# Optimization experiments

Measured on AMD Instinct MI355X. Metric: run time of the kernel, lower is better.

Reference implementation:

```python
import jax, jax.numpy as jnp
import numpy as np

B, T, D, P, M = 4, 1024, 512, 64, 256


def setup_inputs() -> dict:
    key = jax.random.key(0)
    ks = jax.random.split(key, 10)
    s_d = 1.0 / np.sqrt(D)
    s_m = 1.0 / np.sqrt(M)
    s_p = 1.0 / np.sqrt(P)
    return {
        "inputs": jax.random.normal(ks[0], (B, T, D), dtype=jnp.float32),
        "ec": jax.random.normal(ks[1], (B, M), dtype=jnp.float32),
        "W1": jax.random.uniform(ks[2], (D, P), jnp.float32, -s_d, s_d),
        "b1": jax.random.uniform(ks[3], (P,), jnp.float32, -s_d, s_d),
        "W2": jax.random.uniform(ks[4], (D, P), jnp.float32, -s_d, s_d),
        "b2": jax.random.uniform(ks[5], (P,), jnp.float32, -s_d, s_d),
        "W3": jax.random.uniform(ks[6], (M, P), jnp.float32, -s_m, s_m),
        "b3": jax.random.uniform(ks[7], (P,), jnp.float32, -s_m, s_m),
        "wa_w": jax.random.uniform(ks[8], (P,), jnp.float32, -s_p, s_p),
        "wa_b": jax.random.uniform(ks[9], (), jnp.float32, -s_p, s_p),
    }


def reference(inputs, ec, W1, b1, W2, b2, W3, b3, wa_w, wa_b):
    # inputs: (B,T,D), ec: (B,M)
    w1h = inputs @ W1 + b1          # (B,T,P)
    w2h = inputs @ W2 + b2          # (B,T,P)
    w3e = ec @ W3 + b3              # (B,P)
    # Gt: (B,T,T,P) via broadcast add + tanh
    gt = jnp.tanh(w1h[:, :, None, :] + w2h[:, None, :, :] + w3e[:, None, None, :])
    at = jnp.einsum('btup,p->btu', gt, wa_w) + wa_b   # (B,T,T)
    at = jax.nn.softmax(at, axis=-1)
    out = jnp.einsum('btu,bud->btd', at, inputs)      # (B,T,D)
    return out
```

## Files before the change

kernel.cpp:

```cpp
#include <hip/hip_runtime.h>
#include <hip/hip_bf16.h>

constexpr int BB = 4;
constexpr int TT = 1024;
constexpr int DD = 512;
constexpr int PP = 64;
constexpr int MM = 256;

constexpr float CSCALE = 2.8853900817779268f;
constexpr float L2E = 1.4426950408889634f;

typedef __attribute__((ext_vector_type(8))) short v8s;
typedef __attribute__((ext_vector_type(4))) float v4f;
typedef __attribute__((ext_vector_type(2))) float v2f;
typedef unsigned int __attribute__((address_space(1))) gu32;
typedef unsigned int __attribute__((address_space(3))) su32;

__device__ __forceinline__ unsigned short f2bf(float f) {
    unsigned u = __builtin_bit_cast(unsigned, f);
    unsigned r = (u + 0x7fffu + ((u >> 16) & 1u)) >> 16;
    return (unsigned short)r;
}
__device__ __forceinline__ float bf2f(unsigned short h) {
    return __builtin_bit_cast(float, (unsigned)h << 16);
}
__device__ __forceinline__ void split2(float v, unsigned short& h, unsigned short& l) {
    unsigned short hh = f2bf(v);
    h = hh;
    l = f2bf(v - bf2f(hh));
}
__device__ __forceinline__ void gld_lds16(const void* g, void* l) {
    __builtin_amdgcn_global_load_lds((const gu32*)g, (su32*)l, 16, 0, 0);
}
__device__ __forceinline__ v2f pfma(v2f a, v2f b, v2f c) {
    return __builtin_elementwise_fma(a, b, c);
}

__global__ __launch_bounds__(256) void prep1_kernel(
    const float* __restrict__ x, const float* __restrict__ ec,
    const float* __restrict__ W1, const float* __restrict__ W2,
    const float* __restrict__ W3, const float* __restrict__ b3,
    unsigned short* __restrict__ xt,
    unsigned short* __restrict__ WhT, unsigned short* __restrict__ WlT,
    float* __restrict__ E3) {
    __shared__ float tile[64][65];
    int bid = blockIdx.x;
    int tid = threadIdx.x;
    if (bid < 512) {
        int d0 = (bid & 7) << 6;
        int u0 = ((bid >> 3) & 15) << 6;
        int b = bid >> 7;
        int c4 = (tid & 15) << 2, r = tid >> 4;
        #pragma unroll
        for (int i = 0; i < 4; i++) {
            int row = r + (i << 4);
            float4 v = *(const float4*)(x + ((size_t)b * TT + u0 + row) * DD + d0 + c4);
            tile[row][c4 + 0] = v.x;
            tile[row][c4 + 1] = v.y;
            tile[row][c4 + 2] = v.z;
            tile[row][c4 + 3] = v.w;
        }
        __syncthreads();
        int dd = tid >> 2;
        int uq = (tid & 3) << 4;
        unsigned short us[16];
        #pragma unroll
        for (int j = 0; j < 16; j++) us[j] = f2bf(tile[uq + j][dd]);
        uint4 w0, w1;
        w0.x = us[0] | ((unsigned)us[1] << 16);  w0.y = us[2] | ((unsigned)us[3] << 16);
        w0.z = us[4] | ((unsigned)us[5] << 16);  w0.w = us[6] | ((unsigned)us[7] << 16);
        w1.x = us[8] | ((unsigned)us[9] << 16);  w1.y = us[10] | ((unsigned)us[11] << 16);
        w1.z = us[12] | ((unsigned)us[13] << 16); w1.w = us[14] | ((unsigned)us[15] << 16);
        unsigned short* dst = xt + ((size_t)b * DD + d0 + dd) * TT + u0 + uq;
        *(uint4*)dst = w0;
        *(uint4*)(dst + 8) = w1;
    } else if (bid < 528) {
        int w = bid - 512;
        int n = tid >> 1;
        int kb = (w << 5) + ((tid & 1) << 4);
        unsigned short hs[16], ls[16];
        #pragma unroll
        for (int kk = 0; kk < 16; kk++) {
            int k = kb + kk;
            float v = (n < 64) ? W1[k * PP + n] : W2[k * PP + (n - 64)];
            split2(v, hs[kk], ls[kk]);
        }
        uint4 a, bqq;
        a.x = hs[0] | ((unsigned)hs[1] << 16);   a.y = hs[2] | ((unsigned)hs[3] << 16);
        a.z = hs[4] | ((unsigned)hs[5] << 16);   a.w = hs[6] | ((unsigned)hs[7] << 16);
        bqq.x = hs[8] | ((unsigned)hs[9] << 16); bqq.y = hs[10] | ((unsigned)hs[11] << 16);
        bqq.z = hs[12] | ((unsigned)hs[13] << 16); bqq.w = hs[14] | ((unsigned)hs[15] << 16);
        *(uint4*)(WhT + (size_t)n * DD + kb) = a;
        *(uint4*)(WhT + (size_t)n * DD + kb + 8) = bqq;
        a.x = ls[0] | ((unsigned)ls[1] << 16);   a.y = ls[2] | ((unsigned)ls[3] << 16);
        a.z = ls[4] | ((unsigned)ls[5] << 16);   a.w = ls[6] | ((unsigned)ls[7] << 16);
        bqq.x = ls[8] | ((unsigned)ls[9] << 16); bqq.y = ls[10] | ((unsigned)ls[11] << 16);
        bqq.z = ls[12] | ((unsigned)ls[13] << 16); bqq.w = ls[14] | ((unsigned)ls[15] << 16);
        *(uint4*)(WlT + (size_t)n * DD + kb) = a;
        *(uint4*)(WlT + (size_t)n * DD + kb + 8) = bqq;
    } else {
        int b = tid >> 6, p = tid & 63;
        float a = b3[p];
        const float* e = ec + (size_t)b * MM;
        #pragma unroll 4
        for (int m = 0; m < MM; m++) a = fmaf(e[m], W3[m * PP + p], a);
        E3[b * PP + p] = __builtin_amdgcn_exp2f(a * CSCALE);
    }
}

__global__ __launch_bounds__(256) void prep2_kernel(
    const float* __restrict__ x,
    const unsigned short* __restrict__ WhT, const unsigned short* __restrict__ WlT,
    const float* __restrict__ b1, const float* __restrict__ b2,
    float* __restrict__ E1, float* __restrict__ E2) {
    __shared__ unsigned short AsH[16][72];
    __shared__ unsigned short AsL[16][72];
    __shared__ unsigned short BsH[128][72];
    __shared__ unsigned short BsL[128][72];
    int m0 = blockIdx.x << 4;
    int tid = threadIdx.x;
    int lane = tid & 63;
    int wv = tid >> 6;
    int wn = wv << 5;
    int l15 = lane & 15;
    int quad = lane >> 4;

    v4f acc[2];
    acc[0] = (v4f){0.f, 0.f, 0.f, 0.f};
    acc[1] = acc[0];

    for (int k0 = 0; k0 < DD; k0 += 64) {
        __syncthreads();
        {
            int row = tid >> 4, k4 = (tid & 15) << 2;
            float4 v = *(const float4*)(x + (size_t)(m0 + row) * DD + k0 + k4);
            unsigned short h0, h1, h2, h3, l0, l1, l2, l3;
            split2(v.x, h0, l0); split2(v.y, h1, l1);
            split2(v.z, h2, l2); split2(v.w, h3, l3);
            uint2 hw, lw;
            hw.x = h0 | ((unsigned)h1 << 16); hw.y = h2 | ((unsigned)h3 << 16);
            lw.x = l0 | ((unsigned)l1 << 16); lw.y = l2 | ((unsigned)l3 << 16);
            *(uint2*)&AsH[row][k4] = hw;
            *(uint2*)&AsL[row][k4] = lw;
        }
        #pragma unroll
        for (int i = 0; i < 4; i++) {
            int s = (i << 8) + tid;
            int row = s >> 3, k8 = (s & 7) << 3;
            *(uint4*)&BsH[row][k8] = *(const uint4*)(WhT + (size_t)row * DD + k0 + k8);
            *(uint4*)&BsL[row][k8] = *(const uint4*)(WlT + (size_t)row * DD + k0 + k8);
        }
        __syncthreads();
        #pragma unroll
        for (int kk = 0; kk < 64; kk += 32) {
            int kc = kk + (quad << 3);
            v8s aH0 = *(const v8s*)&AsH[l15][kc];
            v8s aL0 = *(const v8s*)&AsL[l15][kc];
            #pragma unroll
            for (int nt = 0; nt < 2; nt++) {
                v8s bH = *(const v8s*)&BsH[wn + (nt << 4) + l15][kc];
                v8s bL = *(const v8s*)&BsL[wn + (nt << 4) + l15][kc];
                acc[nt] = __builtin_amdgcn_mfma_f32_16x16x32_bf16(aH0, bH, acc[nt], 0, 0, 0);
                acc[nt] = __builtin_amdgcn_mfma_f32_16x16x32_bf16(aH0, bL, acc[nt], 0, 0, 0);
                acc[nt] = __builtin_amdgcn_mfma_f32_16x16x32_bf16(aL0, bH, acc[nt], 0, 0, 0);
            }
        }
    }
    #pragma unroll
    for (int nt = 0; nt < 2; nt++) {
        int n = wn + (nt << 4) + l15;
        int p = n & 63;
        float bias = (n < 64) ? b1[p] : b2[p];
        float* E = (n < 64) ? E1 : E2;
        int rbase = m0 + (quad << 2);
        #pragma unroll
        for (int r = 0; r < 4; r++) {
            float h = acc[nt][r] + bias;
            E[(size_t)(rbase + r) * PP + p] = __builtin_amdgcn_exp2f(h * CSCALE);
        }
    }
}

__global__ __launch_bounds__(256, 4) void scores_kernel(
    const float* __restrict__ E1, const float* __restrict__ E2,
    const float* __restrict__ E3, const float* __restrict__ wa_w,
    const float* __restrict__ wa_b, unsigned short* __restrict__ at_bf) {
    __shared__ float sm[4][4];
    __shared__ float sl[4][4];
    int tid = threadIdx.x;
    int bid = blockIdx.x;
    int b = bid >> 8;
    int t0 = (bid & 255) << 2;
    int pp = tid & 7;
    int uu = tid >> 3;
    int p0 = pp << 3;
    int lane = tid & 63;
    int wv = tid >> 6;
    int my_i = pp & 3;
    bool pbit1 = (pp & 2) != 0;
    bool pbit0 = (pp & 1) != 0;

    v2f ww2p[8];
    v2f Hp[2][8];
    float base;
    {
        float4 wv0 = *(const float4*)(wa_w + p0);
        float4 wv1 = *(const float4*)(wa_w + p0 + 4);
        float s = wv0.x + wv0.y + wv0.z + wv0.w + wv1.x + wv1.y + wv1.z + wv1.w;
        s += __shfl_xor(s, 1, 64);
        s += __shfl_xor(s, 2, 64);
        s += __shfl_xor(s, 4, 64);
        base = (s + wa_b[0]) * L2E;
        float ww2[8];
        ww2[0] = -2.f * L2E * wv0.x; ww2[1] = -2.f * L2E * wv0.y;
        ww2[2] = -2.f * L2E * wv0.z; ww2[3] = -2.f * L2E * wv0.w;
        ww2[4] = -2.f * L2E * wv1.x; ww2[5] = -2.f * L2E * wv1.y;
        ww2[6] = -2.f * L2E * wv1.z; ww2[7] = -2.f * L2E * wv1.w;
        #pragma unroll
        for (int j = 0; j < 8; j++) ww2p[j] = (v2f){ww2[j], ww2[j]};
        float4 e3a = *(const float4*)(E3 + (b << 6) + p0);
        float4 e3b = *(const float4*)(E3 + (b << 6) + p0 + 4);
        float H[4][8];
        #pragma unroll
        for (int i = 0; i < 4; i++) {
            const float* e1p = E1 + (((size_t)(b << 10) + t0 + i) << 6) + p0;
            float4 a = *(const float4*)e1p;
            float4 c = *(const float4*)(e1p + 4);
            H[i][0] = a.x * e3a.x; H[i][1] = a.y * e3a.y; H[i][2] = a.z * e3a.z; H[i][3] = a.w * e3a.w;
            H[i][4] = c.x * e3b.x; H[i][5] = c.y * e3b.y; H[i][6] = c.z * e3b.z; H[i][7] = c.w * e3b.w;
        }
        #pragma unroll
        for (int pr = 0; pr < 2; pr++)
            #pragma unroll
            for (int j = 0; j < 8; j++)
                Hp[pr][j] = (v2f){H[2 * pr][j], H[2 * pr + 1][j]};
    }
    const v2f one2 = (v2f){1.0f, 1.0f};

    float own[32];
    float mown = -1e30f;
    #pragma unroll
    for (int k = 0; k < 32; k++) {
        int u = (k << 5) + uu;
        const float* ep = E2 + (((size_t)(b << 10) + u) << 6) + p0;
        float4 e0 = *(const float4*)ep;
        float4 e1 = *(const float4*)(ep + 4);
        v2f evp[8];
        evp[0] = (v2f){e0.x, e0.x}; evp[1] = (v2f){e0.y, e0.y};
        evp[2] = (v2f){e0.z, e0.z}; evp[3] = (v2f){e0.w, e0.w};
        evp[4] = (v2f){e1.x, e1.x}; evp[5] = (v2f){e1.y, e1.y};
        evp[6] = (v2f){e1.z, e1.z}; evp[7] = (v2f){e1.w, e1.w};
        float sr_[4];
        #pragma unroll
        for (int pr = 0; pr < 2; pr++) {
            v2f d0 = pfma(Hp[pr][0], evp[0], one2);
            v2f d1 = pfma(Hp[pr][1], evp[1], one2);
            v2f d2 = pfma(Hp[pr][2], evp[2], one2);
            v2f d3 = pfma(Hp[pr][3], evp[3], one2);
            v2f d4 = pfma(Hp[pr][4], evp[4], one2);
            v2f d5 = pfma(Hp[pr][5], evp[5], one2);
            v2f d6 = pfma(Hp[pr][6], evp[6], one2);
            v2f d7 = pfma(Hp[pr][7], evp[7], one2);
            v2f e01 = d0 * d1, e23 = d2 * d3, e45 = d4 * d5, e67 = d6 * d7;
            v2f n01 = pfma(ww2p[0], d1, ww2p[1] * d0);
            v2f n23 = pfma(ww2p[2], d3, ww2p[3] * d2);
            v2f n45 = pfma(ww2p[4], d5, ww2p[5] * d4);
            v2f n67 = pfma(ww2p[6], d7, ww2p[7] * d6);
            v2f q03 = e01 * e23, q47 = e45 * e67;
            v2f n03 = pfma(n23, e01, n01 * e23);
            v2f n47 = pfma(n67, e45, n45 * e67);
            v2f Dq = q03 * q47;
            v2f Nq = pfma(n47, q03, n03 * q47);
            sr_[2 * pr]     = Nq.x * __builtin_amdgcn_rcpf(Dq.x);
            sr_[2 * pr + 1] = Nq.y * __builtin_amdgcn_rcpf(Dq.y);
        }
        float s0 = sr_[0], s1 = sr_[1], s2 = sr_[2], s3 = sr_[3];
        s0 += __shfl_xor(s0, 4, 64);
        s1 += __shfl_xor(s1, 4, 64);
        s2 += __shfl_xor(s2, 4, 64);
        s3 += __shfl_xor(s3, 4, 64);
        float op0 = pbit1 ? s2 : s0;
        float op1 = pbit1 ? s3 : s1;
        float ot0 = pbit1 ? s0 : s2;
        float ot1 = pbit1 ? s1 : s3;
        op0 += __shfl_xor(ot0, 2, 64);
        op1 += __shfl_xor(ot1, 2, 64);
        float osel = pbit0 ? op1 : op0;
        float osnd = pbit0 ? op0 : op1;
        osel += __shfl_xor(osnd, 1, 64);
        float o = osel + base;
        own[k] = o;
        mown = fmaxf(mown, o);
    }
    mown = fmaxf(mown, __shfl_xor(mown, 8, 64));
    mown = fmaxf(mown, __shfl_xor(mown, 16, 64));
    mown = fmaxf(mown, __shfl_xor(mown, 32, 64));
    if (lane < 4) sm[wv][lane] = mown;
    __syncthreads();
    float mx = fmaxf(fmaxf(sm[0][my_i], sm[1][my_i]), fmaxf(sm[2][my_i], sm[3][my_i]));

    float l = 0.f;
    #pragma unroll
    for (int k = 0; k < 32; k++) {
        float e = __builtin_amdgcn_exp2f(own[k] - mx);
        own[k] = e;
        l += e;
    }
    l += __shfl_xor(l, 8, 64);
    l += __shfl_xor(l, 16, 64);
    l += __shfl_xor(l, 32, 64);
    if (lane < 4) sl[wv][lane] = l;
    __syncthreads();
    float inv = 1.0f / (sl[0][my_i] + sl[1][my_i] + sl[2][my_i] + sl[3][my_i]);

    if (pp < 4) {
        size_t rowbase = ((size_t)((b << 10) + t0 + my_i)) << 10;
        #pragma unroll
        for (int k = 0; k < 32; k++) {
            at_bf[rowbase + (k << 5) + uu] = f2bf(own[k] * inv);
        }
    }
}

__global__ __launch_bounds__(256) void av_mfma_kernel(
    const unsigned short* __restrict__ at_bf, const unsigned short* __restrict__ xt,
    float* __restrict__ out) {
    __shared__ unsigned short As[64 * 64];
    __shared__ unsigned short Bs[64 * 64];
    int b = blockIdx.z;
    int m0 = blockIdx.y << 6;
    int n0 = blockIdx.x << 6;
    const unsigned short* A = at_bf + ((size_t)b << 20);
    const unsigned short* Bt = xt + (size_t)b * DD * TT;
    int tid = threadIdx.x;
    int lane = tid & 63;
    int wv = tid >> 6;
    int wm = (wv & 1) << 5;
    int wn = (wv >> 1) << 5;
    int l15 = lane & 15;
    int quad = lane >> 4;

    int sr = lane >> 3;
    int scg = (lane & 7) ^ sr;

    v4f acc00 = {0.f, 0.f, 0.f, 0.f}, acc01 = acc00, acc10 = acc00, acc11 = acc00;

    for (int k0 = 0; k0 < TT; k0 += 64) {
        __syncthreads();
        #pragma unroll
        for (int t = 0; t < 2; t++) {
            int r0 = (wv << 4) + (t << 3);
            int row = r0 + sr;
            gld_lds16(A + (size_t)(m0 + row) * TT + k0 + (scg << 3), &As[r0 << 6]);
            gld_lds16(Bt + (size_t)(n0 + row) * TT + k0 + (scg << 3), &Bs[r0 << 6]);
        }
        __syncthreads();
        #pragma unroll
        for (int kq = 0; kq < 2; kq++) {
            int c = (kq << 2) + quad;
            int swz = (c ^ (l15 & 7)) << 3;
            v8s a0 = *(const v8s*)&As[((wm + l15) << 6) + swz];
            v8s a1 = *(const v8s*)&As[((wm + 16 + l15) << 6) + swz];
            v8s b0 = *(const v8s*)&Bs[((wn + l15) << 6) + swz];
            v8s b1 = *(const v8s*)&Bs[((wn + 16 + l15) << 6) + swz];
            acc00 = __builtin_amdgcn_mfma_f32_16x16x32_bf16(a0, b0, acc00, 0, 0, 0);
            acc01 = __builtin_amdgcn_mfma_f32_16x16x32_bf16(a0, b1, acc01, 0, 0, 0);
            acc10 = __builtin_amdgcn_mfma_f32_16x16x32_bf16(a1, b0, acc10, 0, 0, 0);
            acc11 = __builtin_amdgcn_mfma_f32_16x16x32_bf16(a1, b1, acc11, 0, 0, 0);
        }
    }
    float* C = out + (size_t)b * TT * DD;
    int rbase = m0 + wm + (quad << 2);
    int cn = n0 + wn + l15;
    #pragma unroll
    for (int r = 0; r < 4; r++) {
        C[(size_t)(rbase + r) * DD + cn]           = acc00[r];
        C[(size_t)(rbase + r) * DD + cn + 16]      = acc01[r];
        C[(size_t)(rbase + 16 + r) * DD + cn]      = acc10[r];
        C[(size_t)(rbase + 16 + r) * DD + cn + 16] = acc11[r];
    }
}

extern "C" void kernel_launch(void* const* d_in, const int* in_sizes, int n_in,
                              void* d_out, int out_size, void* d_ws, size_t ws_size,
                              hipStream_t stream) {
    const float* inputs = (const float*)d_in[0];
    const float* ec     = (const float*)d_in[1];
    const float* W1     = (const float*)d_in[2];
    const float* b1     = (const float*)d_in[3];
    const float* W2     = (const float*)d_in[4];
    const float* b2     = (const float*)d_in[5];
    const float* W3     = (const float*)d_in[6];
    const float* b3     = (const float*)d_in[7];
    const float* wa_w   = (const float*)d_in[8];
    const float* wa_b   = (const float*)d_in[9];
    float* out = (float*)d_out;

    float* ws = (float*)d_ws;
    float* E1 = ws;
    float* E2 = ws + 262144;
    float* E3 = ws + 524288;
    unsigned short* at_bf = (unsigned short*)(ws + 524800);
    unsigned short* xt    = (unsigned short*)(ws + 524800 + 2097152);
    unsigned short* WhT   = at_bf;
    unsigned short* WlT   = at_bf + 65536;

    hipLaunchKernelGGL(prep1_kernel, dim3(529), dim3(256), 0, stream,
                       inputs, ec, W1, W2, W3, b3, xt, WhT, WlT, E3);
    hipLaunchKernelGGL(prep2_kernel, dim3(256), dim3(256), 0, stream,
                       inputs, WhT, WlT, b1, b2, E1, E2);
    hipLaunchKernelGGL(scores_kernel, dim3(1024), dim3(256), 0, stream,
                       E1, E2, E3, wa_w, wa_b, at_bf);
    hipLaunchKernelGGL(av_mfma_kernel, dim3(DD / 64, TT / 64, BB), dim3(256), 0, stream,
                       at_bf, xt, out);
}
```

Baseline: 145.2 us.

## Process eight query rows per block in scores kernel to reuse E2 loads

Each scores block now handles 8 query rows instead of 4, so every E2 row loaded is reused across twice as many queries, and the grid is halved. The cross-lane reduction is extended to a three-stage butterfly over 8 partial sums, and all 8 p-lanes now write output rows instead of only half. Register pressure grows (Hp doubles), so launch bounds drop to 2 blocks per SM, which lowers occupancy.

```diff
diff --git a/kernel.cpp b/kernel.cpp
--- a/kernel.cpp
+++ b/kernel.cpp
@@ -181,27 +181,27 @@
     }
 }
 
-__global__ __launch_bounds__(256, 4) void scores_kernel(
+__global__ __launch_bounds__(256, 2) void scores_kernel(
     const float* __restrict__ E1, const float* __restrict__ E2,
     const float* __restrict__ E3, const float* __restrict__ wa_w,
     const float* __restrict__ wa_b, unsigned short* __restrict__ at_bf) {
-    __shared__ float sm[4][4];
-    __shared__ float sl[4][4];
+    __shared__ float sm[4][8];
+    __shared__ float sl[4][8];
     int tid = threadIdx.x;
     int bid = blockIdx.x;
-    int b = bid >> 8;
-    int t0 = (bid & 255) << 2;
+    int b = bid >> 7;
+    int t0 = (bid & 127) << 3;
     int pp = tid & 7;
     int uu = tid >> 3;
     int p0 = pp << 3;
     int lane = tid & 63;
     int wv = tid >> 6;
-    int my_i = pp & 3;
-    bool pbit1 = (pp & 2) != 0;
-    bool pbit0 = (pp & 1) != 0;
+    bool pb0 = (pp & 1) != 0;
+    bool pb1 = (pp & 2) != 0;
+    bool pb2 = (pp & 4) != 0;
 
     v2f ww2p[8];
-    v2f Hp[2][8];
+    v2f Hp[4][8];
     float base;
     {
         float4 wv0 = *(const float4*)(wa_w + p0);
@@ -220,20 +220,21 @@
         for (int j = 0; j < 8; j++) ww2p[j] = (v2f){ww2[j], ww2[j]};
         float4 e3a = *(const float4*)(E3 + (b << 6) + p0);
         float4 e3b = *(const float4*)(E3 + (b << 6) + p0 + 4);
-        float H[4][8];
-        #pragma unroll
-        for (int i = 0; i < 4; i++) {
-            const float* e1p = E1 + (((size_t)(b << 10) + t0 + i) << 6) + p0;
-            float4 a = *(const float4*)e1p;
-            float4 c = *(const float4*)(e1p + 4);
-            H[i][0] = a.x * e3a.x; H[i][1] = a.y * e3a.y; H[i][2] = a.z * e3a.z; H[i][3] = a.w * e3a.w;
-            H[i][4] = c.x * e3b.x; H[i][5] = c.y * e3b.y; H[i][6] = c.z * e3b.z; H[i][7] = c.w * e3b.w;
-        }
-        #pragma unroll
-        for (int pr = 0; pr < 2; pr++)
+        float e3[8] = {e3a.x, e3a.y, e3a.z, e3a.w, e3b.x, e3b.y, e3b.z, e3b.w};
+        #pragma unroll
+        for (int q = 0; q < 4; q++) {
+            const float* r0p = E1 + (((size_t)(b << 10) + t0 + 2 * q) << 6) + p0;
+            const float* r1p = r0p + PP;
+            float4 a0 = *(const float4*)r0p;
+            float4 a1 = *(const float4*)(r0p + 4);
+            float4 c0 = *(const float4*)r1p;
+            float4 c1 = *(const float4*)(r1p + 4);
+            float r0v[8] = {a0.x, a0.y, a0.z, a0.w, a1.x, a1.y, a1.z, a1.w};
+            float r1v[8] = {c0.x, c0.y, c0.z, c0.w, c1.x, c1.y, c1.z, c1.w};
             #pragma unroll
             for (int j = 0; j < 8; j++)
-                Hp[pr][j] = (v2f){H[2 * pr][j], H[2 * pr + 1][j]};
+                Hp[q][j] = (v2f){r0v[j] * e3[j], r1v[j] * e3[j]};
+        }
     }
     const v2f one2 = (v2f){1.0f, 1.0f};
 
@@ -250,17 +251,17 @@
         evp[2] = (v2f){e0.z, e0.z}; evp[3] = (v2f){e0.w, e0.w};
         evp[4] = (v2f){e1.x, e1.x}; evp[5] = (v2f){e1.y, e1.y};
         evp[6] = (v2f){e1.z, e1.z}; evp[7] = (v2f){e1.w, e1.w};
-        float sr_[4];
-        #pragma unroll
-        for (int pr = 0; pr < 2; pr++) {
-            v2f d0 = pfma(Hp[pr][0], evp[0], one2);
-            v2f d1 = pfma(Hp[pr][1], evp[1], one2);
-            v2f d2 = pfma(Hp[pr][2], evp[2], one2);
-            v2f d3 = pfma(Hp[pr][3], evp[3], one2);
-            v2f d4 = pfma(Hp[pr][4], evp[4], one2);
-            v2f d5 = pfma(Hp[pr][5], evp[5], one2);
-            v2f d6 = pfma(Hp[pr][6], evp[6], one2);
-            v2f d7 = pfma(Hp[pr][7], evp[7], one2);
+        float sr_[8];
+        #pragma unroll
+        for (int q = 0; q < 4; q++) {
+            v2f d0 = pfma(Hp[q][0], evp[0], one2);
+            v2f d1 = pfma(Hp[q][1], evp[1], one2);
+            v2f d2 = pfma(Hp[q][2], evp[2], one2);
+            v2f d3 = pfma(Hp[q][3], evp[3], one2);
+            v2f d4 = pfma(Hp[q][4], evp[4], one2);
+            v2f d5 = pfma(Hp[q][5], evp[5], one2);
+            v2f d6 = pfma(Hp[q][6], evp[6], one2);
+            v2f d7 = pfma(Hp[q][7], evp[7], one2);
             v2f e01 = d0 * d1, e23 = d2 * d3, e45 = d4 * d5, e67 = d6 * d7;
             v2f n01 = pfma(ww2p[0], d1, ww2p[1] * d0);
             v2f n23 = pfma(ww2p[2], d3, ww2p[3] * d2);
@@ -271,33 +272,40 @@
             v2f n47 = pfma(n67, e45, n45 * e67);
             v2f Dq = q03 * q47;
             v2f Nq = pfma(n47, q03, n03 * q47);
-            sr_[2 * pr]     = Nq.x * __builtin_amdgcn_rcpf(Dq.x);
-            sr_[2 * pr + 1] = Nq.y * __builtin_amdgcn_rcpf(Dq.y);
-        }
-        float s0 = sr_[0], s1 = sr_[1], s2 = sr_[2], s3 = sr_[3];
-        s0 += __shfl_xor(s0, 4, 64);
-        s1 += __shfl_xor(s1, 4, 64);
-        s2 += __shfl_xor(s2, 4, 64);
-        s3 += __shfl_xor(s3, 4, 64);
-        float op0 = pbit1 ? s2 : s0;
-        float op1 = pbit1 ? s3 : s1;
-        float ot0 = pbit1 ? s0 : s2;
-        float ot1 = pbit1 ? s1 : s3;
-        op0 += __shfl_xor(ot0, 2, 64);
-        op1 += __shfl_xor(ot1, 2, 64);
-        float osel = pbit0 ? op1 : op0;
-        float osnd = pbit0 ? op0 : op1;
-        osel += __shfl_xor(osnd, 1, 64);
-        float o = osel + base;
+            sr_[2 * q]     = Nq.x * __builtin_amdgcn_rcpf(Dq.x);
+            sr_[2 * q + 1] = Nq.y * __builtin_amdgcn_rcpf(Dq.y);
+        }
+        float a0 = pb2 ? sr_[4] : sr_[0];
+        float a1 = pb2 ? sr_[5] : sr_[1];
+        float a2 = pb2 ? sr_[6] : sr_[2];
+        float a3 = pb2 ? sr_[7] : sr_[3];
+        float o0 = pb2 ? sr_[0] : sr_[4];
+        float o1 = pb2 ? sr_[1] : sr_[5];
+        float o2 = pb2 ? sr_[2] : sr_[6];
+        float o3 = pb2 ? sr_[3] : sr_[7];
+        a0 += __shfl_xor(o0, 4, 64);
+        a1 += __shfl_xor(o1, 4, 64);
+        a2 += __shfl_xor(o2, 4, 64);
+        a3 += __shfl_xor(o3, 4, 64);
+        float b0v = pb1 ? a2 : a0;
+        float b1v = pb1 ? a3 : a1;
+        float t0_ = pb1 ? a0 : a2;
+        float t1_ = pb1 ? a1 : a3;
+        b0v += __shfl_xor(t0_, 2, 64);
+        b1v += __shfl_xor(t1_, 2, 64);
+        float c0 = pb0 ? b1v : b0v;
+        float c1 = pb0 ? b0v : b1v;
+        c0 += __shfl_xor(c1, 1, 64);
+        float o = c0 + base;
         own[k] = o;
         mown = fmaxf(mown, o);
     }
     mown = fmaxf(mown, __shfl_xor(mown, 8, 64));
     mown = fmaxf(mown, __shfl_xor(mown, 16, 64));
     mown = fmaxf(mown, __shfl_xor(mown, 32, 64));
-    if (lane < 4) sm[wv][lane] = mown;
+    if (lane < 8) sm[wv][lane] = mown;
     __syncthreads();
-    float mx = fmaxf(fmaxf(sm[0][my_i], sm[1][my_i]), fmaxf(sm[2][my_i], sm[3][my_i]));
+    float mx = fmaxf(fmaxf(sm[0][pp], sm[1][pp]), fmaxf(sm[2][pp], sm[3][pp]));
 
     float l = 0.f;
     #pragma unroll
@@ -309,12 +317,12 @@
     l += __shfl_xor(l, 8, 64);
     l += __shfl_xor(l, 16, 64);
     l += __shfl_xor(l, 32, 64);
-    if (lane < 4) sl[wv][lane] = l;
+    if (lane < 8) sl[wv][lane] = l;
     __syncthreads();
-    float inv = 1.0f / (sl[0][my_i] + sl[1][my_i] + sl[2][my_i] + sl[3][my_i]);
-
-    if (pp < 4) {
-        size_t rowbase = ((size_t)((b << 10) + t0 + my_i)) << 10;
+    float inv = 1.0f / (sl[0][pp] + sl[1][pp] + sl[2][pp] + sl[3][pp]);
+
+    {
+        size_t rowbase = ((size_t)((b << 10) + t0 + pp)) << 10;
         #pragma unroll
         for (int k = 0; k < 32; k++) {
             at_bf[rowbase + (k << 5) + uu] = f2bf(own[k] * inv);
@@ -409,7 +417,7 @@
                        inputs, ec, W1, W2, W3, b3, xt, WhT, WlT, E3);
     hipLaunchKernelGGL(prep2_kernel, dim3(256), dim3(256), 0, stream,
                        inputs, WhT, WlT, b1, b2, E1, E2);
-    hipLaunchKernelGGL(scores_kernel, dim3(1024), dim3(256), 0, stream,
+    hipLaunchKernelGGL(scores_kernel, dim3(512), dim3(256), 0, stream,
                        E1, E2, E3, wa_w, wa_b, at_bf);
     hipLaunchKernelGGL(av_mfma_kernel, dim3(DD / 64, TT / 64, BB), dim3(256), 0, stream,
                        at_bf, xt, out);
```

Result: no change. 145.5 us (+0.2%).
